# Performance work log

Hardware: AMD Instinct MI355X
Metric: run time of the kernel (lower is better)

Reference implementation:

```python
import jax, jax.numpy as jnp
import numpy as np
from jax import lax

CURRICULUM_EP = 12
LI, LS, LW = 0.5, 0.8, 3.0


def _gauss_win(ws, C, dtype):
    coords = jnp.arange(ws, dtype=jnp.float32) - ws // 2
    g = jnp.exp(-coords ** 2 / (2 * 1.5 ** 2))
    win = g[None, :] * g[:, None]
    win = win / win.sum()
    # depthwise kernel, OIHW with I=1, O=C
    return jnp.broadcast_to(win[None, None], (C, 1, ws, ws)).astype(dtype)


def _dwconv(x, win, p, C):
    return lax.conv_general_dilated(
        x, win, window_strides=(1, 1), padding=[(p, p), (p, p)],
        dimension_numbers=('NCHW', 'OIHW', 'NCHW'), feature_group_count=C)


def diff_ssim(x, y, ws=11):
    C1, C2 = 0.01 ** 2, 0.03 ** 2
    C = x.shape[1]
    p = ws // 2
    win = _gauss_win(ws, C, x.dtype)
    mx = _dwconv(x, win, p, C)
    my = _dwconv(y, win, p, C)
    sxx = _dwconv(x * x, win, p, C) - mx ** 2
    syy = _dwconv(y * y, win, p, C) - my ** 2
    sxy = _dwconv(x * y, win, p, C) - mx * my
    ssim_map = (2 * mx * my + C1) * (2 * sxy + C2) / ((mx ** 2 + my ** 2 + C1) * (sxx + syy + C2))
    return ssim_map.mean()


def setup_inputs() -> dict:
    key = jax.random.key(0)
    k1, k2, k3, k4 = jax.random.split(key, 4)
    B, C, H, W = 16, 3, 512, 512
    NB = 1024  # watermark bits
    eps = 1e-4
    cover = jax.random.uniform(k1, (B, C, H, W), dtype=jnp.float32)
    wmed = jax.random.uniform(k2, (B, C, H, W), dtype=jnp.float32)
    wm_orig = jax.random.uniform(k3, (B, NB), dtype=jnp.float32)
    wm_ext = jnp.clip(jax.random.uniform(k4, (B, NB), dtype=jnp.float32), eps, 1.0 - eps)
    return {"cover": cover, "wmed": wmed, "wm_orig": wm_orig, "wm_ext": wm_ext, "epoch": 20}


def reference(cover, wmed, wm_orig, wm_ext, epoch):
    ml = jnp.mean((wmed - cover) ** 2)
    sv = diff_ssim(wmed, cover)
    sl = 1.0 - sv
    wl = jnp.mean(-(wm_orig * jnp.log(wm_ext) + (1.0 - wm_orig) * jnp.log(1.0 - wm_ext)))
    if epoch <= CURRICULUM_EP:
        w_img, w_ssim = 0.05, 0.05
    else:
        progress = min(1.0, (epoch - CURRICULUM_EP) / 10.0)
        w_img = 0.05 + (LI - 0.05) * progress
        w_ssim = 0.05 + (LS - 0.05) * progress
    total = w_img * ml + w_ssim * sl + LW * wl
    return (total, ml, sv, wl)
```

## Files before the change

### kernel.cpp

```cpp
#include <hip/hip_runtime.h>
#include <math.h>

#define H_IMG 512
#define W_IMG 512
#define TH 32
#define TW 32
#define HALO 5
#define WS11 11
#define SH (TH + 2*HALO)
#define NTHREADS 256
#define TPB 4

#define RS 36
#define RBUF_N (5*SH*RS)

typedef float f2 __attribute__((ext_vector_type(2)));

__host__ __device__ constexpr float WT(int t) {
    return (t==0||t==10) ? 0.00102838f :
           (t==1||t==9)  ? 0.00759873f :
           (t==2||t==8)  ? 0.03600075f :
           (t==3||t==7)  ? 0.10936070f :
           (t==4||t==6)  ? 0.21300556f :
           (t==5)        ? 0.26601172f : 0.0f;
}

static __device__ __forceinline__ f2 splat2(float v) { f2 r = {v, v}; return r; }

__global__ __launch_bounds__(NTHREADS, 4) void ssim_mse_tile(
        const float* __restrict__ cover, const float* __restrict__ wmed,
        float* __restrict__ part, int nParts) {
    __shared__ __align__(16) float rbuf[RBUF_N];
    __shared__ float red[8];

    const int tid = threadIdx.x;
    float ssim_acc = 0.f, mse_acc = 0.f;

    for (int it = 0; it < TPB; ++it) {
        const int tile = blockIdx.x * TPB + it;
        const int bx = tile & 15;
        const int by = (tile >> 4) & 15;
        const int pl = tile >> 8;
        const size_t pbase = (size_t)pl * (H_IMG*W_IMG);
        const float* xp = wmed + pbase;
        const float* yp = cover + pbase;
        const int ty0 = by*TH - HALO;
        const int tx0 = bx*TW - HALO;
        const bool xin = (bx != 0) && (bx != 15);

        for (int t = tid; t < SH*8; t += NTHREADS) {
            const int r = t >> 3, c0 = (t & 7) << 2;
            const int gy = ty0 + r;
            const bool rok = (unsigned)gy < (unsigned)H_IMG;
            float xv[14], yv[14];
            if (rok && xin) {
                const int ga = tx0 + c0 - 3;
                const float* rx = xp + (size_t)gy*W_IMG + ga;
                const float* ry = yp + (size_t)gy*W_IMG + ga;
                float4 XA = *(const float4*)(rx);
                float4 XB = *(const float4*)(rx + 4);
                float4 XC = *(const float4*)(rx + 8);
                float4 XD = *(const float4*)(rx + 12);
                float  XE = rx[16];
                float4 YA = *(const float4*)(ry);
                float4 YB = *(const float4*)(ry + 4);
                float4 YC = *(const float4*)(ry + 8);
                float4 YD = *(const float4*)(ry + 12);
                float  YE = ry[16];
                xv[0]=XA.w;  xv[1]=XB.x;  xv[2]=XB.y;  xv[3]=XB.z;  xv[4]=XB.w;
                xv[5]=XC.x;  xv[6]=XC.y;  xv[7]=XC.z;  xv[8]=XC.w;  xv[9]=XD.x;
                xv[10]=XD.y; xv[11]=XD.z; xv[12]=XD.w; xv[13]=XE;
                yv[0]=YA.w;  yv[1]=YB.x;  yv[2]=YB.y;  yv[3]=YB.z;  yv[4]=YB.w;
                yv[5]=YC.x;  yv[6]=YC.y;  yv[7]=YC.z;  yv[8]=YC.w;  yv[9]=YD.x;
                yv[10]=YD.y; yv[11]=YD.z; yv[12]=YD.w; yv[13]=YE;
            } else if (rok) {
                const int gc = tx0 + c0;
                const float* prx = xp + (size_t)gy*W_IMG + gc;
                const float* pry = yp + (size_t)gy*W_IMG + gc;
#pragma unroll
                for (int j = 0; j < 14; ++j) {
                    bool ok = (unsigned)(gc + j) < (unsigned)W_IMG;
                    xv[j] = ok ? prx[j] : 0.f;
                    yv[j] = ok ? pry[j] : 0.f;
                }
            } else {
#pragma unroll
                for (int j = 0; j < 14; ++j) { xv[j] = 0.f; yv[j] = 0.f; }
            }

            if (rok && r >= HALO && r < HALO+TH) {
#pragma unroll
                for (int j = 5; j < 9; ++j) {
                    float d = xv[j] - yv[j];
                    mse_acc = fmaf(d, d, mse_acc);
                }
            }

            f2 A[5][2];
#pragma unroll
            for (int f = 0; f < 5; ++f) { A[f][0] = splat2(0.f); A[f][1] = splat2(0.f); }
#pragma unroll
            for (int j = 0; j < 14; ++j) {
                float px = xv[j], py = yv[j];
                float pxx = px*px, pyy = py*py, pxy = px*py;
#pragma unroll
                for (int p = 0; p < 2; ++p) {
                    const int t0 = j - 2*p;
                    if (t0 >= 0 && t0 <= WS11) {
                        const f2 wp = {WT(t0), WT(t0-1)};
                        A[0][p] = __builtin_elementwise_fma(wp, splat2(px),  A[0][p]);
                        A[1][p] = __builtin_elementwise_fma(wp, splat2(py),  A[1][p]);
                        A[2][p] = __builtin_elementwise_fma(wp, splat2(pxx), A[2][p]);
                        A[3][p] = __builtin_elementwise_fma(wp, splat2(pyy), A[3][p]);
                        A[4][p] = __builtin_elementwise_fma(wp, splat2(pxy), A[4][p]);
                    }
                }
            }
            float* wb = &rbuf[r*RS + c0];
#pragma unroll
            for (int f = 0; f < 5; ++f) {
                *(float4*)(wb + f*SH*RS) =
                    make_float4(A[f][0].x, A[f][0].y, A[f][1].x, A[f][1].y);
            }
        }
        __syncthreads();

        if (((tid >> 7) & 1) == (it & 1)) {
            const f2 c1 = {0.01f*0.01f, 0.01f*0.01f};
            const f2 c2 = {0.03f*0.03f, 0.03f*0.03f};
            const f2 two = {2.f, 2.f};
            const int s  = tid & 127;
            const int c  = s & 31;
            const int r0 = (s >> 5) << 3;
            f2 acc2[5][4];
#pragma unroll
            for (int f = 0; f < 5; ++f)
#pragma unroll
                for (int p = 0; p < 4; ++p) acc2[f][p] = splat2(0.f);
#pragma unroll
            for (int f = 0; f < 5; ++f) {
                const float* rb = &rbuf[f*SH*RS + r0*RS + c];
#pragma unroll
                for (int i = 0; i < 18; ++i) {
                    float v = rb[i*RS];
#pragma unroll
                    for (int p = 0; p < 4; ++p) {
                        const int t0 = i - 2*p;
                        if (t0 >= 0 && t0 <= WS11) {
                            const f2 wp = {WT(t0), WT(t0-1)};
                            acc2[f][p] = __builtin_elementwise_fma(wp, splat2(v), acc2[f][p]);
                        }
                    }
                }
            }
#pragma unroll
            for (int p = 0; p < 4; ++p) {
                f2 mx = acc2[0][p], my = acc2[1][p];
                f2 sxx = acc2[2][p] - mx*mx;
                f2 syy = acc2[3][p] - my*my;
                f2 sxy = acc2[4][p] - mx*my;
                f2 num = (two*mx*my + c1) * (two*sxy + c2);
                f2 den = (mx*mx + my*my + c1) * (sxx + syy + c2);
                ssim_acc += __fdividef(num.x, den.x) + __fdividef(num.y, den.y);
            }
        }
        __syncthreads();
    }

#pragma unroll
    for (int off = 32; off > 0; off >>= 1) {
        ssim_acc += __shfl_down(ssim_acc, off);
        mse_acc  += __shfl_down(mse_acc, off);
    }
    int wid = tid >> 6, lane = tid & 63;
    if (lane == 0) { red[wid] = ssim_acc; red[4+wid] = mse_acc; }
    __syncthreads();
    if (tid == 0) {
        float s = red[0]+red[1]+red[2]+red[3];
        float m = red[4]+red[5]+red[6]+red[7];
        part[blockIdx.x] = s;
        part[nParts + blockIdx.x] = m;
    }
}

#define FT 1024
__global__ __launch_bounds__(FT) void finalize_k(
        const float* __restrict__ part, int nParts,
        const float* __restrict__ wm_orig, const float* __restrict__ wm_ext,
        int nWm, const int* __restrict__ epoch_p,
        float* __restrict__ out, double inv_npix, double inv_nwm) {
    __shared__ double red[48];
    int tid = threadIdx.x;
    double s_ssim = 0.0, s_mse = 0.0, s_wl = 0.0;
    const float4* s4 = (const float4*)part;
    const float4* m4 = (const float4*)(part + nParts);
    int n4 = nParts >> 2;
    for (int i = tid; i < n4; i += FT) {
        float4 v = s4[i];
        s_ssim += (double)((v.x + v.y) + (v.z + v.w));
        float4 u = m4[i];
        s_mse  += (double)((u.x + u.y) + (u.z + u.w));
    }
    const float4* p4 = (const float4*)wm_orig;
    const float4* q4 = (const float4*)wm_ext;
    int w4 = nWm >> 2;
    for (int i = tid; i < w4; i += FT) {
        float4 p = p4[i], q = q4[i];
        float a;
        a  = -(p.x*__logf(q.x) + (1.f-p.x)*__logf(1.f-q.x));
        a += -(p.y*__logf(q.y) + (1.f-p.y)*__logf(1.f-q.y));
        a += -(p.z*__logf(q.z) + (1.f-p.z)*__logf(1.f-q.z));
        a += -(p.w*__logf(q.w) + (1.f-p.w)*__logf(1.f-q.w));
        s_wl += (double)a;
    }
#pragma unroll
    for (int off = 32; off > 0; off >>= 1) {
        s_ssim += __shfl_down(s_ssim, off);
        s_mse  += __shfl_down(s_mse, off);
        s_wl   += __shfl_down(s_wl, off);
    }
    int wid = tid >> 6, lane = tid & 63;
    if (lane == 0) { red[wid] = s_ssim; red[16+wid] = s_mse; red[32+wid] = s_wl; }
    __syncthreads();
    if (tid == 0) {
        double ssim_sum = 0.0, mse_sum = 0.0, wl_sum = 0.0;
        for (int i = 0; i < 16; ++i) {
            ssim_sum += red[i]; mse_sum += red[16+i]; wl_sum += red[32+i];
        }
        float sv = (float)(ssim_sum * inv_npix);
        float ml = (float)(mse_sum  * inv_npix);
        float wl = (float)(wl_sum   * inv_nwm);
        int e = *epoch_p;
        float w_img, w_ssim;
        if (e <= 12) {
            w_img = 0.05f; w_ssim = 0.05f;
        } else {
            float progress = fminf(1.0f, (float)(e - 12) / 10.0f);
            w_img  = 0.05f + (0.5f - 0.05f)*progress;
            w_ssim = 0.05f + (0.8f - 0.05f)*progress;
        }
        float sl = 1.0f - sv;
        float total = w_img*ml + w_ssim*sl + 3.0f*wl;
        out[0] = total;
        out[1] = ml;
        out[2] = sv;
        out[3] = wl;
    }
}

extern "C" void kernel_launch(void* const* d_in, const int* in_sizes, int n_in,
                              void* d_out, int out_size, void* d_ws, size_t ws_size,
                              hipStream_t stream) {
    const float* cover   = (const float*)d_in[0];
    const float* wmed    = (const float*)d_in[1];
    const float* wm_orig = (const float*)d_in[2];
    const float* wm_ext  = (const float*)d_in[3];
    const int*   epoch   = (const int*)d_in[4];
    float* out = (float*)d_out;

    int npix   = in_sizes[0];
    int planes = npix / (H_IMG * W_IMG);
    int nWm    = in_sizes[2];

    int nTiles  = 16 * 16 * planes;
    int nBlocks = nTiles / TPB;
    int nParts  = nBlocks;
    float* part = (float*)d_ws;

    ssim_mse_tile<<<nBlocks, NTHREADS, 0, stream>>>(cover, wmed, part, nParts);
    finalize_k<<<1, FT, 0, stream>>>(part, nParts, wm_orig, wm_ext, nWm,
                                     epoch, out,
                                     1.0 / (double)npix, 1.0 / (double)nWm);
}
```

Baseline: 180.8 us.

## Stream tall vertical strips through a shared-memory ring buffer to reuse halo rows

Each block now walks a 32-wide, 256-row strip in four 64-row chunks and keeps horizontally filtered rows in a 75-row ring buffer. Halo rows are then computed once per strip instead of once per 32x32 tile. The vertical pass is also remapped so all 256 threads work on every chunk, each handling 2 columns by 4 rows, rather than half the threads idling in alternate iterations. The cost is more shared memory, lower occupancy (launch bounds 3), and fewer blocks (16*2*planes = 1536).

```diff
diff --git a/kernel.cpp b/kernel.cpp
--- a/kernel.cpp
+++ b/kernel.cpp
@@ -3,16 +3,16 @@
 
 #define H_IMG 512
 #define W_IMG 512
-#define TH 32
 #define TW 32
+#define CH 64
+#define NCHUNK 4
+#define STRIP (CH*NCHUNK)
 #define HALO 5
 #define WS11 11
-#define SH (TH + 2*HALO)
+#define RING 75
+#define RS 36
+#define FSTR (RING*RS)
 #define NTHREADS 256
-#define TPB 4
-
-#define RS 36
-#define RBUF_N (5*SH*RS)
 
 typedef float f2 __attribute__((ext_vector_type(2)));
 
@@ -27,30 +27,34 @@
 
 static __device__ __forceinline__ f2 splat2(float v) { f2 r = {v, v}; return r; }
 
-__global__ __launch_bounds__(NTHREADS, 4) void ssim_mse_tile(
+__global__ __launch_bounds__(NTHREADS, 3) void ssim_mse_tile(
         const float* __restrict__ cover, const float* __restrict__ wmed,
         float* __restrict__ part, int nParts) {
-    __shared__ __align__(16) float rbuf[RBUF_N];
-    __shared__ float red[8];
+    __shared__ __align__(16) float rbuf[5*FSTR];
 
     const int tid = threadIdx.x;
+    const int bx  = blockIdx.x & 15;
+    const int ys  = (blockIdx.x >> 4) & 1;
+    const int pl  = blockIdx.x >> 5;
+    const size_t pbase = (size_t)pl * (H_IMG*W_IMG);
+    const float* xp = wmed + pbase;
+    const float* yp = cover + pbase;
+    const int Y0  = ys << 8;
+    const int tx0 = bx*TW - HALO;
+    const bool xin = (bx != 0) && (bx != 15);
+
     float ssim_acc = 0.f, mse_acc = 0.f;
 
-    for (int it = 0; it < TPB; ++it) {
-        const int tile = blockIdx.x * TPB + it;
-        const int bx = tile & 15;
-        const int by = (tile >> 4) & 15;
-        const int pl = tile >> 8;
-        const size_t pbase = (size_t)pl * (H_IMG*W_IMG);
-        const float* xp = wmed + pbase;
-        const float* yp = cover + pbase;
-        const int ty0 = by*TH - HALO;
-        const int tx0 = bx*TW - HALO;
-        const bool xin = (bx != 0) && (bx != 15);
-
-        for (int t = tid; t < SH*8; t += NTHREADS) {
-            const int r = t >> 3, c0 = (t & 7) << 2;
-            const int gy = ty0 + r;
+    for (int k = 0; k < NCHUNK; ++k) {
+        const int nrows = (k == 0) ? (CH + 2*HALO) : CH;
+        const int hr0   = (k == 0) ? -HALO : (CH*k + HALO);
+        const int ntask = nrows << 3;
+
+        for (int t = tid; t < ntask; t += NTHREADS) {
+            const int r  = t >> 3, c0 = (t & 7) << 2;
+            const int hr = hr0 + r;
+            const int gy = Y0 + hr;
+            const int slot = (hr + HALO) % RING;
             const bool rok = (unsigned)gy < (unsigned)H_IMG;
             float xv[14], yv[14];
             if (rok && xin) {
@@ -88,7 +92,7 @@
                 for (int j = 0; j < 14; ++j) { xv[j] = 0.f; yv[j] = 0.f; }
             }
 
-            if (rok && r >= HALO && r < HALO+TH) {
+            if ((unsigned)hr < (unsigned)STRIP) {
 #pragma unroll
                 for (int j = 5; j < 9; ++j) {
                     float d = xv[j] - yv[j];
@@ -116,51 +120,51 @@
                     }
                 }
             }
-            float* wb = &rbuf[r*RS + c0];
+            float* wb = &rbuf[slot*RS + c0];
 #pragma unroll
             for (int f = 0; f < 5; ++f) {
-                *(float4*)(wb + f*SH*RS) =
+                *(float4*)(wb + f*FSTR) =
                     make_float4(A[f][0].x, A[f][0].y, A[f][1].x, A[f][1].y);
             }
         }
         __syncthreads();
 
-        if (((tid >> 7) & 1) == (it & 1)) {
-            const f2 c1 = {0.01f*0.01f, 0.01f*0.01f};
-            const f2 c2 = {0.03f*0.03f, 0.03f*0.03f};
+        {
+            const int cb = (tid & 15) << 1;
+            const int g  = tid >> 4;
+            int sb = (CH*k + (g << 2)) % RING;
+            f2 acc[5][4];
+#pragma unroll
+            for (int f = 0; f < 5; ++f)
+#pragma unroll
+                for (int o = 0; o < 4; ++o) acc[f][o] = splat2(0.f);
+            const float* bp = rbuf + cb;
+#pragma unroll
+            for (int i = 0; i < 14; ++i) {
+                int sl = sb + i; if (sl >= RING) sl -= RING;
+                const float* rp = bp + sl*RS;
+#pragma unroll
+                for (int f = 0; f < 5; ++f) {
+                    f2 v = *(const f2*)(rp + f*FSTR);
+#pragma unroll
+                    for (int o = 0; o < 4; ++o) {
+                        const int tp = i - o;
+                        if (tp >= 0 && tp <= 10)
+                            acc[f][o] = __builtin_elementwise_fma(splat2(WT(tp)), v, acc[f][o]);
+                    }
+                }
+            }
+            const f2 c1v = {1e-4f, 1e-4f};
+            const f2 c2v = {9e-4f, 9e-4f};
             const f2 two = {2.f, 2.f};
-            const int s  = tid & 127;
-            const int c  = s & 31;
-            const int r0 = (s >> 5) << 3;
-            f2 acc2[5][4];
-#pragma unroll
-            for (int f = 0; f < 5; ++f)
-#pragma unroll
-                for (int p = 0; p < 4; ++p) acc2[f][p] = splat2(0.f);
-#pragma unroll
-            for (int f = 0; f < 5; ++f) {
-                const float* rb = &rbuf[f*SH*RS + r0*RS + c];
-#pragma unroll
-                for (int i = 0; i < 18; ++i) {
-                    float v = rb[i*RS];
-#pragma unroll
-                    for (int p = 0; p < 4; ++p) {
-                        const int t0 = i - 2*p;
-                        if (t0 >= 0 && t0 <= WS11) {
-                            const f2 wp = {WT(t0), WT(t0-1)};
-                            acc2[f][p] = __builtin_elementwise_fma(wp, splat2(v), acc2[f][p]);
-                        }
-                    }
-                }
-            }
-#pragma unroll
-            for (int p = 0; p < 4; ++p) {
-                f2 mx = acc2[0][p], my = acc2[1][p];
-                f2 sxx = acc2[2][p] - mx*mx;
-                f2 syy = acc2[3][p] - my*my;
-                f2 sxy = acc2[4][p] - mx*my;
-                f2 num = (two*mx*my + c1) * (two*sxy + c2);
-                f2 den = (mx*mx + my*my + c1) * (sxx + syy + c2);
+#pragma unroll
+            for (int o = 0; o < 4; ++o) {
+                f2 mx = acc[0][o], my = acc[1][o];
+                f2 sxx = acc[2][o] - mx*mx;
+                f2 syy = acc[3][o] - my*my;
+                f2 sxy = acc[4][o] - mx*my;
+                f2 num = (two*mx*my + c1v) * (two*sxy + c2v);
+                f2 den = (mx*mx + my*my + c1v) * (sxx + syy + c2v);
                 ssim_acc += __fdividef(num.x, den.x) + __fdividef(num.y, den.y);
             }
         }
@@ -172,14 +176,12 @@
         ssim_acc += __shfl_down(ssim_acc, off);
         mse_acc  += __shfl_down(mse_acc, off);
     }
-    int wid = tid >> 6, lane = tid & 63;
-    if (lane == 0) { red[wid] = ssim_acc; red[4+wid] = mse_acc; }
+    const int wid = tid >> 6, lane = tid & 63;
+    if (lane == 0) { rbuf[wid] = ssim_acc; rbuf[4+wid] = mse_acc; }
     __syncthreads();
     if (tid == 0) {
-        float s = red[0]+red[1]+red[2]+red[3];
-        float m = red[4]+red[5]+red[6]+red[7];
-        part[blockIdx.x] = s;
-        part[nParts + blockIdx.x] = m;
+        part[blockIdx.x] = rbuf[0]+rbuf[1]+rbuf[2]+rbuf[3];
+        part[nParts + blockIdx.x] = rbuf[4]+rbuf[5]+rbuf[6]+rbuf[7];
     }
 }
 
@@ -262,8 +264,7 @@
     int planes = npix / (H_IMG * W_IMG);
     int nWm    = in_sizes[2];
 
-    int nTiles  = 16 * 16 * planes;
-    int nBlocks = nTiles / TPB;
+    int nBlocks = 16 * 2 * planes;
     int nParts  = nBlocks;
     float* part = (float*)d_ws;
 
```

Result: slower. 190.4 us (+5.4%).
